# Kernel optimization log

Measured on AMD Instinct MI355X. Metric: run time of the kernel, lower is better.

The kernel has to match this reference:

```python
import jax, jax.numpy as jnp
import numpy as np

IMG_FEAT = 2048
HIDDEN = 1024
K_TIMES = 3
GLIMPSE = 8
BA_HIDDEN = K_TIMES * HIDDEN  # 3072


def setup_inputs() -> dict:
    key = jax.random.key(0)
    ks = jax.random.split(key, 9)
    b, n_v, n_q = 64, 128, 32
    v = jax.random.normal(ks[0], (b, n_v, IMG_FEAT), dtype=jnp.float32)
    q = jax.random.normal(ks[1], (b, n_q, HIDDEN), dtype=jnp.float32)
    # weight-normed Linear params (weight_norm with dim=None -> scalar g)
    v_w = jax.random.normal(ks[2], (BA_HIDDEN, IMG_FEAT), dtype=jnp.float32) * 0.02
    v_g = jnp.asarray(jnp.linalg.norm(v_w), dtype=jnp.float32)
    v_b = jnp.zeros((BA_HIDDEN,), dtype=jnp.float32)
    q_w = jax.random.normal(ks[3], (BA_HIDDEN, HIDDEN), dtype=jnp.float32) * 0.02
    q_g = jnp.asarray(jnp.linalg.norm(q_w), dtype=jnp.float32)
    q_b = jnp.zeros((BA_HIDDEN,), dtype=jnp.float32)
    h_mat = jax.random.normal(ks[4], (1, GLIMPSE, 1, BA_HIDDEN), dtype=jnp.float32)
    h_bias = jax.random.normal(ks[5], (1, GLIMPSE, 1, 1), dtype=jnp.float32)
    return {"v": v, "q": q, "v_w": v_w, "v_g": v_g, "v_b": v_b,
            "q_w": q_w, "q_g": q_g, "q_b": q_b,
            "h_mat": h_mat, "h_bias": h_bias}


def _wn_linear_relu(x, w, g, b):
    # weight_norm(dim=None): w_eff = g * w / ||w||_F (scalar g)
    w_eff = (g / jnp.linalg.norm(w)) * w
    return jax.nn.relu(jnp.einsum('bnd,kd->bnk', x, w_eff) + b)


def reference(v, q, v_w, v_g, v_b, q_w, q_g, q_b, h_mat, h_bias):
    # dropout layers are identity in eval mode
    v_ = _wn_linear_relu(v, v_w, v_g, v_b)  # [b, n_v, K]
    q_ = _wn_linear_relu(q, q_w, q_g, q_b)  # [b, n_q, K]
    # einsum('xhyk,bvk,bqk->bhvq') with h_mat [1,g,1,K]
    hm = h_mat[0, :, 0, :]  # [g, K]
    logits = jnp.einsum('hk,bvk,bqk->bhvq', hm, v_, q_) + h_bias
    return logits
```

## Files before the change

### kernel.cpp

```cpp
#include <hip/hip_runtime.h>

typedef __attribute__((ext_vector_type(8))) __bf16 bf16x8;
typedef __attribute__((ext_vector_type(4))) float f32x4;
typedef const __attribute__((address_space(1))) unsigned int gas_u32;
typedef __attribute__((address_space(3))) unsigned int las_u32;

__device__ __forceinline__ unsigned short f2bf(float f) {
  unsigned u = __builtin_bit_cast(unsigned, f);
  u = (u + 0x7FFFu + ((u >> 16) & 1u)) >> 16;
  return (unsigned short)u;
}
__device__ __forceinline__ float bf2f(unsigned short h) {
  return __builtin_bit_cast(float, (unsigned)h << 16);
}

__global__ __launch_bounds__(256) void k_sumsq(const float* __restrict__ w, int n4,
                                               float* __restrict__ out) {
  int tid = threadIdx.x;
  float s = 0.f;
  for (int i = blockIdx.x * 256 + tid; i < n4; i += gridDim.x * 256) {
    float4 v = ((const float4*)w)[i];
    s += v.x * v.x + v.y * v.y + v.z * v.z + v.w * v.w;
  }
  for (int off = 32; off; off >>= 1) s += __shfl_down(s, off);
  __shared__ float red[4];
  if ((tid & 63) == 0) red[tid >> 6] = s;
  __syncthreads();
  if (tid == 0) atomicAdd(out, red[0] + red[1] + red[2] + red[3]);
}

__global__ __launch_bounds__(256) void k_cvt(const float* __restrict__ in,
                                             unsigned short* __restrict__ out, int n8) {
  for (int i = blockIdx.x * 256 + threadIdx.x; i < n8; i += gridDim.x * 256) {
    float4 a = ((const float4*)in)[2 * i];
    float4 b = ((const float4*)in)[2 * i + 1];
    uint4 o;
    o.x = f2bf(a.x) | ((unsigned)f2bf(a.y) << 16);
    o.y = f2bf(a.z) | ((unsigned)f2bf(a.w) << 16);
    o.z = f2bf(b.x) | ((unsigned)f2bf(b.y) << 16);
    o.w = f2bf(b.z) | ((unsigned)f2bf(b.w) << 16);
    ((uint4*)out)[i] = o;
  }
}

__global__ __launch_bounds__(512, 2) void k_gemm_wn(
    const unsigned short* __restrict__ A, const unsigned short* __restrict__ B,
    const float* __restrict__ bias, const float* __restrict__ gptr,
    const float* __restrict__ ssptr, unsigned short* __restrict__ C,
    int M, int N, int K, int nbn) {
  __shared__ __align__(16) unsigned short lA[2 * 128 * 64];
  __shared__ __align__(16) unsigned short lB[2 * 384 * 64];
  const int tid = threadIdx.x;
  const int wid = tid >> 6, lane = tid & 63;
  const int l15 = lane & 15, l4 = lane >> 4;
  const int wm = wid >> 2, wn = wid & 3;
  const int rr = tid >> 3;
  const int scol = ((tid & 7) ^ (rr & 7)) << 3;

  int nwg = gridDim.x;
  int wg = (blockIdx.x & 7) * (nwg >> 3) + (blockIdx.x >> 3);
  int bm = wg / nbn, bn = wg % nbn;

  const unsigned short* Ab = A + (size_t)bm * 128 * K;
  const unsigned short* Bb = B + (size_t)bn * 384 * K;
  const int nt = K >> 6;

#define STAGEU(U, TS)                                                            \
  {                                                                              \
    int ts_ = (TS) < nt ? (TS) : nt - 1;                                         \
    if ((U) < 2) {                                                               \
      __builtin_amdgcn_global_load_lds(                                          \
          (gas_u32*)(Ab + (size_t)((U)*64 + rr) * K + ts_ * 64 + scol),          \
          (las_u32*)(lA + ((TS)&1) * 8192 + (U)*4096 + tid * 8), 16, 0, 0);      \
    } else {                                                                     \
      __builtin_amdgcn_global_load_lds(                                          \
          (gas_u32*)(Bb + (size_t)(((U)-2) * 64 + rr) * K + ts_ * 64 + scol),    \
          (las_u32*)(lB + ((TS)&1) * 24576 + ((U)-2) * 4096 + tid * 8), 16, 0,   \
          0);                                                                    \
    }                                                                            \
  }

#define LDSA(DST, MQ, TP)                                                        \
  _Pragma("unroll") for (int i2 = 0; i2 < 2; ++i2) {                             \
    int rl = wm * 64 + ((MQ)*2 + i2) * 16 + l15;                                 \
    const unsigned short* ap = lA + (TP)*8192 + rl * 64;                         \
    int s8 = rl & 7;                                                             \
    DST[i2][0] = *(const bf16x8*)(ap + ((l4 ^ s8) << 3));                        \
    DST[i2][1] = *(const bf16x8*)(ap + (((4 | l4) ^ s8) << 3));                  \
  }

#define LDSB(DST, NQ, TP)                                                        \
  _Pragma("unroll") for (int j3 = 0; j3 < 3; ++j3) {                             \
    int rl = wn * 96 + ((NQ)*3 + j3) * 16 + l15;                                 \
    const unsigned short* bp = lB + (TP)*24576 + rl * 64;                        \
    int s8 = rl & 7;                                                             \
    DST[j3][0] = *(const bf16x8*)(bp + ((l4 ^ s8) << 3));                        \
    DST[j3][1] = *(const bf16x8*)(bp + (((4 | l4) ^ s8) << 3));                  \
  }

#define MFMA12(MQ, NQ, AF, BF)                                                   \
  _Pragma("unroll") for (int ks = 0; ks < 2; ++ks)                               \
  _Pragma("unroll") for (int i2 = 0; i2 < 2; ++i2)                               \
  _Pragma("unroll") for (int j3 = 0; j3 < 3; ++j3)                               \
    acc[(MQ)*2 + i2][(NQ)*3 + j3] = __builtin_amdgcn_mfma_f32_16x16x32_bf16(     \
        AF[i2][ks], BF[j3][ks], acc[(MQ)*2 + i2][(NQ)*3 + j3], 0, 0, 0);

  f32x4 acc[4][6] = {};
  bf16x8 a0_[2][2], a1_[2][2], b0_[3][2], b1_[3][2];

  STAGEU(0, 0) STAGEU(1, 0) STAGEU(2, 0) STAGEU(3, 0)
  STAGEU(4, 0) STAGEU(5, 0) STAGEU(6, 0) STAGEU(7, 0)
  STAGEU(0, 1) STAGEU(1, 1)
  asm volatile("s_waitcnt vmcnt(2)" ::: "memory");
  __builtin_amdgcn_sched_barrier(0);
  __builtin_amdgcn_s_barrier();
  LDSA(a0_, 0, 0)
  STAGEU(2, 1) STAGEU(3, 1)
  LDSB(b0_, 0, 0)

  for (int t = 0; t < nt; ++t) {
    const int cp = t & 1, np = (t + 1) & 1;
    LDSB(b1_, 1, cp)
    STAGEU(4, t + 1) STAGEU(5, t + 1)
    __builtin_amdgcn_s_setprio(1);
    MFMA12(0, 0, a0_, b0_)
    __builtin_amdgcn_s_setprio(0);
    LDSA(a1_, 1, cp)
    STAGEU(6, t + 1) STAGEU(7, t + 1)
    __builtin_amdgcn_s_setprio(1);
    MFMA12(0, 1, a0_, b1_)
    __builtin_amdgcn_s_setprio(0);
    asm volatile("s_waitcnt lgkmcnt(0)" ::: "memory");
    asm volatile("s_waitcnt vmcnt(6)" ::: "memory");
    __builtin_amdgcn_sched_barrier(0);
    __builtin_amdgcn_s_barrier();
    LDSA(a0_, 0, np)
    STAGEU(0, t + 2) STAGEU(1, t + 2)
    __builtin_amdgcn_s_setprio(1);
    MFMA12(1, 0, a1_, b0_)
    __builtin_amdgcn_s_setprio(0);
    asm volatile("s_waitcnt vmcnt(2)" ::: "memory");
    __builtin_amdgcn_sched_barrier(0);
    __builtin_amdgcn_s_barrier();
    LDSB(b0_, 0, np)
    STAGEU(2, t + 2) STAGEU(3, t + 2)
    __builtin_amdgcn_s_setprio(1);
    MFMA12(1, 1, a1_, b1_)
    __builtin_amdgcn_s_setprio(0);
  }

  asm volatile("s_waitcnt vmcnt(0)" ::: "memory");

  float s = gptr[0] / sqrtf(ssptr[0]);
#pragma unroll
  for (int nj = 0; nj < 6; ++nj) {
    int gcol = bn * 384 + wn * 96 + nj * 16 + l15;
    float bv = bias[gcol];
#pragma unroll
    for (int mi = 0; mi < 4; ++mi) {
#pragma unroll
      for (int r = 0; r < 4; ++r) {
        int grow = bm * 128 + wm * 64 + mi * 16 + l4 * 4 + r;
        float v = fmaxf(acc[mi][nj][r] * s + bv, 0.f);
        C[(size_t)grow * N + gcol] = f2bf(v);
      }
    }
  }
#undef STAGEU
#undef LDSA
#undef LDSB
#undef MFMA12
}

__global__ __launch_bounds__(256, 2) void k_gemm_bt(
    const unsigned short* __restrict__ A, const unsigned short* __restrict__ B,
    const float* __restrict__ bias, const float* __restrict__ gptr,
    const float* __restrict__ ssptr, unsigned short* __restrict__ C,
    int M, int N, int K, int nbn) {
  __shared__ __align__(16) unsigned short lA[128 * 64];
  __shared__ __align__(16) unsigned short lB[128 * 64];
  int tid = threadIdx.x;
  int wid = tid >> 6, lane = tid & 63;
  int l15 = lane & 15, l4 = lane >> 4;
  int w0 = wid >> 1, w1 = wid & 1;

  int nwg = gridDim.x;
  int wg = blockIdx.x;
  int cpx = nwg >> 3;
  wg = (wg & 7) * cpx + (wg >> 3);
  int bm = wg / nbn, bn = wg % nbn;

  const unsigned short* Ab = A + (size_t)bm * 128 * K;
  const unsigned short* Bb = B + (size_t)bn * 128 * K;

  f32x4 acc[4][4] = {};

  for (int k0 = 0; k0 < K; k0 += 64) {
    __syncthreads();
#pragma unroll
    for (int i = 0; i < 4; ++i) {
      int ebase = (i * 4 + wid) << 9;
      int eoff = ebase + lane * 8;
      int row = eoff >> 6, col = eoff & 63;
      __builtin_amdgcn_global_load_lds(
          (gas_u32*)(Ab + (size_t)row * K + k0 + col),
          (las_u32*)(lA + ebase), 16, 0, 0);
      __builtin_amdgcn_global_load_lds(
          (gas_u32*)(Bb + (size_t)row * K + k0 + col),
          (las_u32*)(lB + ebase), 16, 0, 0);
    }
    __syncthreads();
#pragma unroll
    for (int ks = 0; ks < 2; ++ks) {
      bf16x8 af[4], bfr[4];
#pragma unroll
      for (int mi = 0; mi < 4; ++mi)
        af[mi] = *(const bf16x8*)(lA + ((w0 * 64 + mi * 16 + l15) * 64 + ks * 32 + l4 * 8));
#pragma unroll
      for (int nj = 0; nj < 4; ++nj)
        bfr[nj] = *(const bf16x8*)(lB + ((w1 * 64 + nj * 16 + l15) * 64 + ks * 32 + l4 * 8));
#pragma unroll
      for (int mi = 0; mi < 4; ++mi)
#pragma unroll
        for (int nj = 0; nj < 4; ++nj)
          acc[mi][nj] =
              __builtin_amdgcn_mfma_f32_16x16x32_bf16(af[mi], bfr[nj], acc[mi][nj], 0, 0, 0);
    }
  }

  float s = gptr[0] / sqrtf(ssptr[0]);
#pragma unroll
  for (int mi = 0; mi < 4; ++mi)
#pragma unroll
    for (int nj = 0; nj < 4; ++nj) {
      int col = bn * 128 + w1 * 64 + nj * 16 + l15;
      float bv = bias[col];
#pragma unroll
      for (int r = 0; r < 4; ++r) {
        int row = bm * 128 + w0 * 64 + mi * 16 + l4 * 4 + r;
        float v = fmaxf(acc[mi][nj][r] * s + bv, 0.f);
        C[(size_t)row * N + col] = f2bf(v);
      }
    }
}

__global__ __launch_bounds__(256, 2) void k_glimpse2(
    const unsigned short* __restrict__ Vh, const unsigned short* __restrict__ Qh,
    const float* __restrict__ hmat, const float* __restrict__ hbias,
    float* __restrict__ out) {
  __shared__ __align__(16) unsigned short lV[128 * 64];
  __shared__ __align__(16) unsigned short lQ[2][32 * 64];
  int tid = threadIdx.x;
  int wid = tid >> 6, lane = tid & 63;
  int l15 = lane & 15, l4 = lane >> 4;

  int id = blockIdx.x;
  int b = id & 63, h2 = id >> 6;

  const unsigned short* Vb = Vh + (size_t)b * 128 * 3072;
  const unsigned short* Qb = Qh + (size_t)b * 32 * 3072;
  const float* hr0 = hmat + h2 * 3072;
  const float* hr1 = hmat + (h2 + 4) * 3072;

  f32x4 acc[2][2][2] = {};

  int eoff = tid * 8;
  int qr = eoff >> 6, qc = eoff & 63;

  for (int k0 = 0; k0 < 3072; k0 += 64) {
    __syncthreads();
#pragma unroll
    for (int i = 0; i < 4; ++i) {
      int ebase = (i * 4 + wid) << 9;
      int eo = ebase + lane * 8;
      int row = eo >> 6, col = eo & 63;
      __builtin_amdgcn_global_load_lds(
          (gas_u32*)(Vb + (size_t)row * 3072 + k0 + col),
          (las_u32*)(lV + ebase), 16, 0, 0);
    }
    {
      uint4 qv = *(const uint4*)(Qb + (size_t)qr * 3072 + k0 + qc);
      float e0 = bf2f((unsigned short)(qv.x & 0xffff)), e1 = bf2f((unsigned short)(qv.x >> 16));
      float e2 = bf2f((unsigned short)(qv.y & 0xffff)), e3 = bf2f((unsigned short)(qv.y >> 16));
      float e4 = bf2f((unsigned short)(qv.z & 0xffff)), e5 = bf2f((unsigned short)(qv.z >> 16));
      float e6 = bf2f((unsigned short)(qv.w & 0xffff)), e7 = bf2f((unsigned short)(qv.w >> 16));
      const float* hp0 = hr0 + k0 + qc;
      const float* hp1 = hr1 + k0 + qc;
      float4 p00 = ((const float4*)hp0)[0], p01 = ((const float4*)hp0)[1];
      float4 p10 = ((const float4*)hp1)[0], p11 = ((const float4*)hp1)[1];
      uint4 o0, o1;
      o0.x = f2bf(e0 * p00.x) | ((unsigned)f2bf(e1 * p00.y) << 16);
      o0.y = f2bf(e2 * p00.z) | ((unsigned)f2bf(e3 * p00.w) << 16);
      o0.z = f2bf(e4 * p01.x) | ((unsigned)f2bf(e5 * p01.y) << 16);
      o0.w = f2bf(e6 * p01.z) | ((unsigned)f2bf(e7 * p01.w) << 16);
      o1.x = f2bf(e0 * p10.x) | ((unsigned)f2bf(e1 * p10.y) << 16);
      o1.y = f2bf(e2 * p10.z) | ((unsigned)f2bf(e3 * p10.w) << 16);
      o1.z = f2bf(e4 * p11.x) | ((unsigned)f2bf(e5 * p11.y) << 16);
      o1.w = f2bf(e6 * p11.z) | ((unsigned)f2bf(e7 * p11.w) << 16);
      *(uint4*)(lQ[0] + eoff) = o0;
      *(uint4*)(lQ[1] + eoff) = o1;
    }
    __syncthreads();
#pragma unroll
    for (int ks = 0; ks < 2; ++ks) {
      bf16x8 af[2];
#pragma unroll
      for (int mi = 0; mi < 2; ++mi)
        af[mi] = *(const bf16x8*)(lV + ((wid * 32 + mi * 16 + l15) * 64 + ks * 32 + l4 * 8));
#pragma unroll
      for (int hh = 0; hh < 2; ++hh) {
        bf16x8 bf2[2];
#pragma unroll
        for (int nj = 0; nj < 2; ++nj)
          bf2[nj] = *(const bf16x8*)(lQ[hh] + ((nj * 16 + l15) * 64 + ks * 32 + l4 * 8));
#pragma unroll
        for (int mi = 0; mi < 2; ++mi)
#pragma unroll
          for (int nj = 0; nj < 2; ++nj)
            acc[hh][mi][nj] = __builtin_amdgcn_mfma_f32_16x16x32_bf16(
                af[mi], bf2[nj], acc[hh][mi][nj], 0, 0, 0);
      }
    }
  }

#pragma unroll
  for (int hh = 0; hh < 2; ++hh) {
    int h = h2 + hh * 4;
    float hb = hbias[h];
    float* ob = out + (size_t)(b * 8 + h) * 128 * 32;
#pragma unroll
    for (int mi = 0; mi < 2; ++mi)
#pragma unroll
      for (int nj = 0; nj < 2; ++nj)
#pragma unroll
        for (int r = 0; r < 4; ++r) {
          int row = wid * 32 + mi * 16 + l4 * 4 + r;
          int col = nj * 16 + l15;
          ob[row * 32 + col] = acc[hh][mi][nj][r] + hb;
        }
  }
}

extern "C" void kernel_launch(void* const* d_in, const int* in_sizes, int n_in,
                              void* d_out, int out_size, void* d_ws, size_t ws_size,
                              hipStream_t stream) {
  const float* v = (const float*)d_in[0];
  const float* q = (const float*)d_in[1];
  const float* v_w = (const float*)d_in[2];
  const float* v_g = (const float*)d_in[3];
  const float* v_b = (const float*)d_in[4];
  const float* q_w = (const float*)d_in[5];
  const float* q_g = (const float*)d_in[6];
  const float* q_b = (const float*)d_in[7];
  const float* hmat = (const float*)d_in[8];
  const float* hbias = (const float*)d_in[9];
  float* out = (float*)d_out;

  const size_t n_v = 16777216;
  const size_t n_vw = 6291456;
  const size_t n_q = 2097152;
  const size_t n_qw = 3145728;
  const size_t n_vh = 25165824;
  const size_t n_qh = 6291456;

  char* ws = (char*)d_ws;
  float* ss = (float*)ws;
  size_t off = 256;
  unsigned short* v_bf = (unsigned short*)(ws + off);  off += n_v * 2;
  unsigned short* vw_bf = (unsigned short*)(ws + off); off += n_vw * 2;
  unsigned short* q_bf = (unsigned short*)(ws + off);  off += n_q * 2;
  unsigned short* qw_bf = (unsigned short*)(ws + off); off += n_qw * 2;
  unsigned short* v_h = (unsigned short*)(ws + off);   off += n_vh * 2;
  unsigned short* q_h = (unsigned short*)(ws + off);   off += n_qh * 2;

  (void)hipMemsetAsync(ss, 0, 8, stream);
  k_sumsq<<<512, 256, 0, stream>>>(v_w, (int)(n_vw / 4), ss + 0);
  k_sumsq<<<512, 256, 0, stream>>>(q_w, (int)(n_qw / 4), ss + 1);

  k_cvt<<<1024, 256, 0, stream>>>(v, v_bf, (int)(n_v / 8));
  k_cvt<<<1024, 256, 0, stream>>>(v_w, vw_bf, (int)(n_vw / 8));
  k_cvt<<<1024, 256, 0, stream>>>(q, q_bf, (int)(n_q / 8));
  k_cvt<<<1024, 256, 0, stream>>>(q_w, qw_bf, (int)(n_qw / 8));

  k_gemm_wn<<<512, 512, 0, stream>>>(v_bf, vw_bf, v_b, v_g, ss + 0, v_h,
                                     8192, 3072, 2048, 8);
  k_gemm_bt<<<384, 256, 0, stream>>>(q_bf, qw_bf, q_b, q_g, ss + 1, q_h,
                                     2048, 3072, 1024, 24);

  k_glimpse2<<<256, 256, 0, stream>>>(v_h, q_h, hmat, hbias, out);
}
```

Before: 237.6 us.

## Restructure V projection GEMM to 256x256 tiles with 8-phase pipelined schedule

Replaces the 128x384-tile V-projection GEMM with a 256x256 tile per workgroup (384 workgroups instead of 512). Each K-step now runs in four quadrant phases, each with its own LDS reads, async global-to-LDS staging and barriers, so that memory traffic overlaps the MFMA work. The square tile raises arithmetic intensity per byte loaded and balances A/B reuse. In exchange there are more barriers per iteration, more accumulator registers (8x4 per wave), and 384 blocks may fill the CUs less evenly.

```diff
diff --git a/kernel.cpp b/kernel.cpp
--- a/kernel.cpp
+++ b/kernel.cpp
@@ -43,133 +43,166 @@
   }
 }
 
-__global__ __launch_bounds__(512, 2) void k_gemm_wn(
+__global__ __launch_bounds__(512, 2) void k_gemm8p(
     const unsigned short* __restrict__ A, const unsigned short* __restrict__ B,
     const float* __restrict__ bias, const float* __restrict__ gptr,
     const float* __restrict__ ssptr, unsigned short* __restrict__ C,
     int M, int N, int K, int nbn) {
-  __shared__ __align__(16) unsigned short lA[2 * 128 * 64];
-  __shared__ __align__(16) unsigned short lB[2 * 384 * 64];
+  __shared__ __align__(16) unsigned short lA[2 * 2 * 8192];
+  __shared__ __align__(16) unsigned short lB[2 * 2 * 8192];
   const int tid = threadIdx.x;
   const int wid = tid >> 6, lane = tid & 63;
   const int l15 = lane & 15, l4 = lane >> 4;
   const int wm = wid >> 2, wn = wid & 3;
-  const int rr = tid >> 3;
-  const int scol = ((tid & 7) ^ (rr & 7)) << 3;
 
   int nwg = gridDim.x;
   int wg = (blockIdx.x & 7) * (nwg >> 3) + (blockIdx.x >> 3);
   int bm = wg / nbn, bn = wg % nbn;
 
-  const unsigned short* Ab = A + (size_t)bm * 128 * K;
-  const unsigned short* Bb = B + (size_t)bn * 384 * K;
+  const unsigned short* Ab = A + (size_t)bm * 256 * K;
+  const unsigned short* Bb = B + (size_t)bn * 256 * K;
   const int nt = K >> 6;
 
-#define STAGEU(U, TS)                                                            \
-  {                                                                              \
-    int ts_ = (TS) < nt ? (TS) : nt - 1;                                         \
-    if ((U) < 2) {                                                               \
-      __builtin_amdgcn_global_load_lds(                                          \
-          (gas_u32*)(Ab + (size_t)((U)*64 + rr) * K + ts_ * 64 + scol),          \
-          (las_u32*)(lA + ((TS)&1) * 8192 + (U)*4096 + tid * 8), 16, 0, 0);      \
-    } else {                                                                     \
-      __builtin_amdgcn_global_load_lds(                                          \
-          (gas_u32*)(Bb + (size_t)(((U)-2) * 64 + rr) * K + ts_ * 64 + scol),    \
-          (las_u32*)(lB + ((TS)&1) * 24576 + ((U)-2) * 4096 + tid * 8), 16, 0,   \
-          0);                                                                    \
-    }                                                                            \
-  }
-
-#define LDSA(DST, MQ, TP)                                                        \
-  _Pragma("unroll") for (int i2 = 0; i2 < 2; ++i2) {                             \
-    int rl = wm * 64 + ((MQ)*2 + i2) * 16 + l15;                                 \
-    const unsigned short* ap = lA + (TP)*8192 + rl * 64;                         \
-    int s8 = rl & 7;                                                             \
-    DST[i2][0] = *(const bf16x8*)(ap + ((l4 ^ s8) << 3));                        \
-    DST[i2][1] = *(const bf16x8*)(ap + (((4 | l4) ^ s8) << 3));                  \
-  }
-
-#define LDSB(DST, NQ, TP)                                                        \
-  _Pragma("unroll") for (int j3 = 0; j3 < 3; ++j3) {                             \
-    int rl = wn * 96 + ((NQ)*3 + j3) * 16 + l15;                                 \
-    const unsigned short* bp = lB + (TP)*24576 + rl * 64;                        \
-    int s8 = rl & 7;                                                             \
-    DST[j3][0] = *(const bf16x8*)(bp + ((l4 ^ s8) << 3));                        \
-    DST[j3][1] = *(const bf16x8*)(bp + (((4 | l4) ^ s8) << 3));                  \
-  }
-
-#define MFMA12(MQ, NQ, AF, BF)                                                   \
-  _Pragma("unroll") for (int ks = 0; ks < 2; ++ks)                               \
-  _Pragma("unroll") for (int i2 = 0; i2 < 2; ++i2)                               \
-  _Pragma("unroll") for (int j3 = 0; j3 < 3; ++j3)                               \
-    acc[(MQ)*2 + i2][(NQ)*3 + j3] = __builtin_amdgcn_mfma_f32_16x16x32_bf16(     \
-        AF[i2][ks], BF[j3][ks], acc[(MQ)*2 + i2][(NQ)*3 + j3], 0, 0, 0);
-
-  f32x4 acc[4][6] = {};
-  bf16x8 a0_[2][2], a1_[2][2], b0_[3][2], b1_[3][2];
-
-  STAGEU(0, 0) STAGEU(1, 0) STAGEU(2, 0) STAGEU(3, 0)
-  STAGEU(4, 0) STAGEU(5, 0) STAGEU(6, 0) STAGEU(7, 0)
-  STAGEU(0, 1) STAGEU(1, 1)
-  asm volatile("s_waitcnt vmcnt(2)" ::: "memory");
+  int ldsoff[2], scolj[2], rowAj[2], rowBj[2];
+#pragma unroll
+  for (int j = 0; j < 2; ++j) {
+    int eoff = (j * 8 + wid) * 512 + lane * 8;
+    int pr = eoff >> 6;
+    int chunk = (eoff >> 3) & 7;
+    ldsoff[j] = eoff;
+    scolj[j] = (chunk ^ (pr & 7)) << 3;
+    rowAj[j] = (pr >> 6) * 128 + (pr & 63);
+    rowBj[j] = (pr >> 5) * 64 + (pr & 31);
+  }
+
+#define STAGE_A(MQ, TS, BUFI)                                                     \
+  {                                                                               \
+    int ts_ = (TS) < nt ? (TS) : nt - 1;                                          \
+    _Pragma("unroll") for (int j = 0; j < 2; ++j) {                               \
+      __builtin_amdgcn_global_load_lds(                                           \
+          (gas_u32*)(Ab + (size_t)(rowAj[j] + (MQ)*64) * K + ts_ * 64 + scolj[j]),\
+          (las_u32*)(lA + (BUFI)*16384 + (MQ)*8192 + ldsoff[j]), 16, 0, 0);       \
+    }                                                                             \
+  }
+
+#define STAGE_B(NQ, TS, BUFI)                                                     \
+  {                                                                               \
+    int ts_ = (TS) < nt ? (TS) : nt - 1;                                          \
+    _Pragma("unroll") for (int j = 0; j < 2; ++j) {                               \
+      __builtin_amdgcn_global_load_lds(                                           \
+          (gas_u32*)(Bb + (size_t)(rowBj[j] + (NQ)*32) * K + ts_ * 64 + scolj[j]),\
+          (las_u32*)(lB + (BUFI)*16384 + (NQ)*8192 + ldsoff[j]), 16, 0, 0);       \
+    }                                                                             \
+  }
+
+#define LDA(DST, MQ, BUFE)                                                        \
+  _Pragma("unroll") for (int mi = 0; mi < 4; ++mi) {                              \
+    int pr = wm * 64 + mi * 16 + l15;                                             \
+    const unsigned short* ap = lA + (BUFE) + (MQ)*8192 + pr * 64;                 \
+    int s8 = pr & 7;                                                              \
+    DST[mi][0] = *(const bf16x8*)(ap + ((l4 ^ s8) << 3));                         \
+    DST[mi][1] = *(const bf16x8*)(ap + (((4 | l4) ^ s8) << 3));                   \
+  }
+
+#define LDB(DST, NQ, BUFE)                                                        \
+  _Pragma("unroll") for (int nj = 0; nj < 2; ++nj) {                              \
+    int pr = wn * 32 + nj * 16 + l15;                                             \
+    const unsigned short* bp = lB + (BUFE) + (NQ)*8192 + pr * 64;                 \
+    int s8 = pr & 7;                                                              \
+    DST[nj][0] = *(const bf16x8*)(bp + ((l4 ^ s8) << 3));                         \
+    DST[nj][1] = *(const bf16x8*)(bp + (((4 | l4) ^ s8) << 3));                   \
+  }
+
+#define MFMAQ(MQ, NQ, AF, BF)                                                     \
+  _Pragma("unroll") for (int ks = 0; ks < 2; ++ks)                                \
+  _Pragma("unroll") for (int mi = 0; mi < 4; ++mi)                                \
+  _Pragma("unroll") for (int nj = 0; nj < 2; ++nj)                                \
+    acc[(MQ)*4 + mi][(NQ)*2 + nj] = __builtin_amdgcn_mfma_f32_16x16x32_bf16(      \
+        AF[mi][ks], BF[nj][ks], acc[(MQ)*4 + mi][(NQ)*2 + nj], 0, 0, 0);
+
+  f32x4 acc[8][4] = {};
+  bf16x8 a0_[4][2], a1_[4][2], b0_[2][2], b1_[2][2];
+
+  STAGE_A(0, 0, 0) STAGE_B(0, 0, 0) STAGE_B(1, 0, 0) STAGE_A(1, 0, 0)
+  STAGE_A(0, 1, 1) STAGE_B(0, 1, 1) STAGE_B(1, 1, 1)
+  asm volatile("s_waitcnt vmcnt(6)" ::: "memory");
   __builtin_amdgcn_sched_barrier(0);
   __builtin_amdgcn_s_barrier();
-  LDSA(a0_, 0, 0)
-  STAGEU(2, 1) STAGEU(3, 1)
-  LDSB(b0_, 0, 0)
 
   for (int t = 0; t < nt; ++t) {
-    const int cp = t & 1, np = (t + 1) & 1;
-    LDSB(b1_, 1, cp)
-    STAGEU(4, t + 1) STAGEU(5, t + 1)
+    const int cbi = t & 1, nbi = cbi ^ 1;
+    const int cb = cbi << 14;
+
+    LDA(a0_, 0, cb)
+    LDB(b0_, 0, cb)
+    STAGE_A(1, t + 1, nbi)
+    asm volatile("s_waitcnt lgkmcnt(8)" ::: "memory");
+    __builtin_amdgcn_sched_barrier(0);
+    __builtin_amdgcn_s_barrier();
+    asm volatile("s_waitcnt lgkmcnt(0)" ::: "memory");
+    __builtin_amdgcn_sched_barrier(0);
     __builtin_amdgcn_s_setprio(1);
-    MFMA12(0, 0, a0_, b0_)
+    MFMAQ(0, 0, a0_, b0_)
     __builtin_amdgcn_s_setprio(0);
-    LDSA(a1_, 1, cp)
-    STAGEU(6, t + 1) STAGEU(7, t + 1)
+    __builtin_amdgcn_s_barrier();
+
+    LDB(b1_, 1, cb)
+    STAGE_A(0, t + 2, cbi)
+    __builtin_amdgcn_sched_barrier(0);
+    __builtin_amdgcn_s_barrier();
+    asm volatile("s_waitcnt lgkmcnt(0)" ::: "memory");
+    __builtin_amdgcn_sched_barrier(0);
     __builtin_amdgcn_s_setprio(1);
-    MFMA12(0, 1, a0_, b1_)
+    MFMAQ(0, 1, a0_, b1_)
     __builtin_amdgcn_s_setprio(0);
+    __builtin_amdgcn_s_barrier();
+
+    LDA(a1_, 1, cb)
+    STAGE_B(0, t + 2, cbi)
+    __builtin_amdgcn_sched_barrier(0);
+    __builtin_amdgcn_s_barrier();
     asm volatile("s_waitcnt lgkmcnt(0)" ::: "memory");
+    __builtin_amdgcn_sched_barrier(0);
+    __builtin_amdgcn_s_setprio(1);
+    MFMAQ(1, 1, a1_, b1_)
+    __builtin_amdgcn_s_setprio(0);
+    __builtin_amdgcn_s_barrier();
+
+    STAGE_B(1, t + 2, cbi)
     asm volatile("s_waitcnt vmcnt(6)" ::: "memory");
     __builtin_amdgcn_sched_barrier(0);
     __builtin_amdgcn_s_barrier();
-    LDSA(a0_, 0, np)
-    STAGEU(0, t + 2) STAGEU(1, t + 2)
     __builtin_amdgcn_s_setprio(1);
-    MFMA12(1, 0, a1_, b0_)
+    MFMAQ(1, 0, a1_, b0_)
     __builtin_amdgcn_s_setprio(0);
-    asm volatile("s_waitcnt vmcnt(2)" ::: "memory");
-    __builtin_amdgcn_sched_barrier(0);
-    __builtin_amdgcn_s_barrier();
-    LDSB(b0_, 0, np)
-    STAGEU(2, t + 2) STAGEU(3, t + 2)
-    __builtin_amdgcn_s_setprio(1);
-    MFMA12(1, 1, a1_, b1_)
-    __builtin_amdgcn_s_setprio(0);
+    __builtin_amdgcn_s_barrier();
   }
 
   asm volatile("s_waitcnt vmcnt(0)" ::: "memory");
 
   float s = gptr[0] / sqrtf(ssptr[0]);
 #pragma unroll
-  for (int nj = 0; nj < 6; ++nj) {
-    int gcol = bn * 384 + wn * 96 + nj * 16 + l15;
-    float bv = bias[gcol];
-#pragma unroll
-    for (int mi = 0; mi < 4; ++mi) {
-#pragma unroll
-      for (int r = 0; r < 4; ++r) {
-        int grow = bm * 128 + wm * 64 + mi * 16 + l4 * 4 + r;
-        float v = fmaxf(acc[mi][nj][r] * s + bv, 0.f);
-        C[(size_t)grow * N + gcol] = f2bf(v);
-      }
-    }
-  }
-#undef STAGEU
-#undef LDSA
-#undef LDSB
-#undef MFMA12
+  for (int nq = 0; nq < 2; ++nq)
+#pragma unroll
+    for (int nj = 0; nj < 2; ++nj) {
+      int gcol = bn * 256 + wn * 64 + nq * 32 + nj * 16 + l15;
+      float bv = bias[gcol];
+#pragma unroll
+      for (int mq = 0; mq < 2; ++mq)
+#pragma unroll
+        for (int mi = 0; mi < 4; ++mi)
+#pragma unroll
+          for (int r = 0; r < 4; ++r) {
+            int grow = bm * 256 + wm * 128 + mq * 64 + mi * 16 + l4 * 4 + r;
+            float v = fmaxf(acc[mq * 4 + mi][nq * 2 + nj][r] * s + bv, 0.f);
+            C[(size_t)grow * N + gcol] = f2bf(v);
+          }
+    }
+#undef STAGE_A
+#undef STAGE_B
+#undef LDA
+#undef LDB
+#undef MFMAQ
 }
 
 __global__ __launch_bounds__(256, 2) void k_gemm_bt(
@@ -309,16 +342,16 @@
         af[mi] = *(const bf16x8*)(lV + ((wid * 32 + mi * 16 + l15) * 64 + ks * 32 + l4 * 8));
 #pragma unroll
       for (int hh = 0; hh < 2; ++hh) {
-        bf16x8 bf2[2];
+        bf16x8 bf2v[2];
 #pragma unroll
         for (int nj = 0; nj < 2; ++nj)
-          bf2[nj] = *(const bf16x8*)(lQ[hh] + ((nj * 16 + l15) * 64 + ks * 32 + l4 * 8));
+          bf2v[nj] = *(const bf16x8*)(lQ[hh] + ((nj * 16 + l15) * 64 + ks * 32 + l4 * 8));
 #pragma unroll
         for (int mi = 0; mi < 2; ++mi)
 #pragma unroll
           for (int nj = 0; nj < 2; ++nj)
             acc[hh][mi][nj] = __builtin_amdgcn_mfma_f32_16x16x32_bf16(
-                af[mi], bf2[nj], acc[hh][mi][nj], 0, 0, 0);
+                af[mi], bf2v[nj], acc[hh][mi][nj], 0, 0, 0);
       }
     }
   }
@@ -382,8 +415,8 @@
   k_cvt<<<1024, 256, 0, stream>>>(q, q_bf, (int)(n_q / 8));
   k_cvt<<<1024, 256, 0, stream>>>(q_w, qw_bf, (int)(n_qw / 8));
 
-  k_gemm_wn<<<512, 512, 0, stream>>>(v_bf, vw_bf, v_b, v_g, ss + 0, v_h,
-                                     8192, 3072, 2048, 8);
+  k_gemm8p<<<384, 512, 0, stream>>>(v_bf, vw_bf, v_b, v_g, ss + 0, v_h,
+                                    8192, 3072, 2048, 12);
   k_gemm_bt<<<384, 256, 0, stream>>>(q_bf, qw_bf, q_b, q_g, ss + 1, q_h,
                                      2048, 3072, 1024, 24);
 
```

New measurement: 284.5 us. 1.2x slower.
